# Performance work log

Hardware: AMD Instinct MI355X
Metric: run time of the kernel (lower is better)

Reference implementation:

```python
import jax, jax.numpy as jnp
import numpy as np

SEQ, EMB, QKV = 4096, 1024, 1024

def setup_inputs() -> dict:
    key = jax.random.key(0)
    k_x, k_q, k_k, k_v = jax.random.split(key, 4)
    scale = 1.0 / np.sqrt(EMB)
    return {
        "x": jax.random.normal(k_x, (SEQ, EMB), dtype=jnp.float32),
        "W_q": jax.random.normal(k_q, (EMB, QKV), dtype=jnp.float32) * scale,
        "W_k": jax.random.normal(k_k, (EMB, QKV), dtype=jnp.float32) * scale,
        "W_v": jax.random.normal(k_v, (EMB, QKV), dtype=jnp.float32) * scale,
    }

def reference(x, W_q, W_k, W_v):
    # Single-head scaled dot-product attention, unbatched: x [S, E]
    d_k = W_q.shape[1]
    Q = x @ W_q          # [S, D]
    K = x @ W_k          # [S, D]
    V = x @ W_v          # [S, D]
    scores = (Q @ K.T) * (1.0 / jnp.sqrt(jnp.asarray(d_k, dtype=x.dtype)))  # [S, S]
    attn = jax.nn.softmax(scores, axis=-1)
    return attn @ V      # [S, D]
```

## Files before the change

kernel.cpp:

```cpp
#include <hip/hip_runtime.h>
#include <cstdint>

#define S_DIM 4096
#define E_DIM 1024
#define D_DIM 1024

typedef __bf16 bf16x8 __attribute__((ext_vector_type(8)));
typedef float  f32x4  __attribute__((ext_vector_type(4)));
typedef unsigned short u16x8 __attribute__((ext_vector_type(8)));

__device__ __forceinline__ unsigned short f2bf(float f) {
  unsigned u = __float_as_uint(f);
  unsigned r = (u + 0x7fffu + ((u >> 16) & 1u)) >> 16;
  return (unsigned short)r;
}

__device__ __forceinline__ void lds_copy16(const unsigned short* g, const unsigned short* l) {
  auto gp = reinterpret_cast<__attribute__((address_space(1))) unsigned int*>(
      reinterpret_cast<uintptr_t>(g));
  auto lp = reinterpret_cast<__attribute__((address_space(3))) unsigned int*>(
      reinterpret_cast<uintptr_t>(l));
  __builtin_amdgcn_global_load_lds(gp, lp, 16, 0, 0);
}

__global__ __launch_bounds__(256) void prep_kernel(
    const float* __restrict__ x,
    const float* __restrict__ Wq, const float* __restrict__ Wk, const float* __restrict__ Wv,
    unsigned short* __restrict__ xbf, unsigned short* __restrict__ Wt,
    float* __restrict__ lsum) {
  const int z = blockIdx.z;
  const int tid = threadIdx.x;
  if (z < 3) {
    const float* W = (z == 0) ? Wq : (z == 1 ? Wk : Wv);
    unsigned short* out = Wt + (size_t)z * E_DIM * D_DIM;
    __shared__ unsigned short tile[32][33];
    int bc = blockIdx.x * 32, br = blockIdx.y * 32;
    int tx = tid & 31, ty = tid >> 5;
#pragma unroll
    for (int i = 0; i < 32; i += 8)
      tile[ty + i][tx] = f2bf(W[(size_t)(br + ty + i) * D_DIM + bc + tx]);
    __syncthreads();
#pragma unroll
    for (int i = 0; i < 32; i += 8)
      out[(size_t)(bc + ty + i) * E_DIM + br + tx] = tile[tx][ty + i];
  } else {
    int bid = blockIdx.y * 32 + blockIdx.x;
    int i = (bid * 256 + tid) * 16;
#pragma unroll
    for (int h = 0; h < 2; h++) {
      float4 a = *(const float4*)(x + i + h * 8);
      float4 b = *(const float4*)(x + i + h * 8 + 4);
      u16x8 o;
      o[0] = f2bf(a.x); o[1] = f2bf(a.y); o[2] = f2bf(a.z); o[3] = f2bf(a.w);
      o[4] = f2bf(b.x); o[5] = f2bf(b.y); o[6] = f2bf(b.z); o[7] = f2bf(b.w);
      *(u16x8*)(xbf + i + h * 8) = o;
    }
    if (bid < 16) lsum[bid * 256 + tid] = 0.f;
  }
}

__global__ __launch_bounds__(256) void transpose_bf16_kernel(
    const unsigned short* __restrict__ in, unsigned short* __restrict__ out,
    int ldin, int ldout) {
  __shared__ unsigned short tile[32][33];
  int bc = blockIdx.x * 32, br = blockIdx.y * 32;
  int tx = threadIdx.x & 31, ty = threadIdx.x >> 5;
#pragma unroll
  for (int i = 0; i < 32; i += 8)
    tile[ty + i][tx] = in[(size_t)(br + ty + i) * ldin + bc + tx];
  __syncthreads();
#pragma unroll
  for (int i = 0; i < 32; i += 8)
    out[(size_t)(bc + ty + i) * ldout + br + tx] = tile[tx][ty + i];
}

template <int MODE, bool SPLIT3>
__global__ __launch_bounds__(256, 2) void gemm_bt_kernel(
    const unsigned short* __restrict__ A, int lda,
    const unsigned short* __restrict__ Bt, int ldb,
    void* __restrict__ Cp, unsigned short* __restrict__ C1,
    unsigned short* __restrict__ C2, int ldc,
    int Kper, float scale, float* __restrict__ lsum) {
  __shared__ __align__(16) unsigned short sA[128 * 64];
  __shared__ __align__(16) unsigned short sB[128 * 64];

  const int tid = threadIdx.x;

  int flat = blockIdx.y * gridDim.x + blockIdx.x;
  int numInG = 8 * gridDim.x;
  int g = flat / numInG;
  int r = flat - g * numInG;
  const int bm = (g * 8 + (r & 7)) * 128;
  const int bn = (r >> 3) * 128;

  const int wave = tid >> 6;
  const int lane = tid & 63;
  const int q    = lane >> 4;
  const int l16  = lane & 15;
  const int wm   = (wave >> 1) * 64;
  const int wn   = (wave & 1) * 64;

  f32x4 zero = {0.f, 0.f, 0.f, 0.f};
  f32x4 acc[4][4];
#pragma unroll
  for (int t = 0; t < 4; t++)
#pragma unroll
    for (int u = 0; u < 4; u++) acc[t][u] = zero;

  const int srow   = tid >> 3;
  const int schunk = (tid & 7) ^ (srow & 3);
  const int kbase  = blockIdx.z * Kper;
  const unsigned short* ap = A  + (size_t)(bm + srow) * lda + kbase + schunk * 8;
  const unsigned short* bp = Bt + (size_t)(bn + srow) * ldb + kbase + schunk * 8;
  unsigned short* saw = sA + wave * 512;
  unsigned short* sbw = sB + wave * 512;
  const size_t stepA = (size_t)32 * lda;
  const size_t stepB = (size_t)32 * ldb;

  const int sw = (q ^ (l16 & 3)) * 8;

  for (int k0 = 0; k0 < Kper; k0 += 64) {
#pragma unroll
    for (int p = 0; p < 4; p++) {
      lds_copy16(ap + k0 + p * stepA, saw + p * 2048);
      lds_copy16(bp + k0 + p * stepB, sbw + p * 2048);
    }
    __syncthreads();

#pragma unroll
    for (int h = 0; h < 2; h++) {
      bf16x8 af[4], bfv[4];
#pragma unroll
      for (int t = 0; t < 4; t++)
        af[t] = *reinterpret_cast<const bf16x8*>(sA + (wm + t * 16 + l16) * 64 + h * 32 + sw);
#pragma unroll
      for (int u = 0; u < 4; u++)
        bfv[u] = *reinterpret_cast<const bf16x8*>(sB + (wn + u * 16 + l16) * 64 + h * 32 + sw);
#pragma unroll
      for (int t = 0; t < 4; t++)
#pragma unroll
        for (int u = 0; u < 4; u++)
          acc[t][u] = __builtin_amdgcn_mfma_f32_16x16x32_bf16(af[t], bfv[u], acc[t][u], 0, 0, 0);
    }
    __syncthreads();
  }

  unsigned short* cb16 = (unsigned short*)Cp;
  int coloff = bn;
  if constexpr (SPLIT3) {
    int which = bn >> 10;
    cb16 = (which == 0) ? (unsigned short*)Cp : (which == 1 ? C1 : C2);
    coloff = bn & 1023;
  }

#pragma unroll
  for (int t = 0; t < 4; t++) {
#pragma unroll
    for (int rr = 0; rr < 4; rr++) {
      const int row = bm + wm + t * 16 + q * 4 + rr;
      float invl = 1.0f;
      if constexpr (MODE == 2) invl = 1.0f / lsum[row];
      float rs = 0.f;
#pragma unroll
      for (int u = 0; u < 4; u++) {
        const int col = coloff + wn + u * 16 + l16;
        float v = acc[t][u][rr] * scale;
        if constexpr (MODE == 0) {
          cb16[(size_t)row * ldc + col] = f2bf(v);
        } else if constexpr (MODE == 1) {
          float p = __expf(v - 8.0f);
          rs += p;
          cb16[(size_t)row * ldc + col] = f2bf(p);
        } else {
          unsafeAtomicAdd((float*)Cp + (size_t)row * ldc + col, acc[t][u][rr] * invl);
        }
      }
      if constexpr (MODE == 1) {
        rs += __shfl_xor(rs, 1);
        rs += __shfl_xor(rs, 2);
        rs += __shfl_xor(rs, 4);
        rs += __shfl_xor(rs, 8);
        if (l16 == 0) unsafeAtomicAdd(&lsum[row], rs);
      }
    }
  }
}

extern "C" void kernel_launch(void* const* d_in, const int* in_sizes, int n_in,
                              void* d_out, int out_size, void* d_ws, size_t ws_size,
                              hipStream_t stream) {
  const float* x  = (const float*)d_in[0];
  const float* Wq = (const float*)d_in[1];
  const float* Wk = (const float*)d_in[2];
  const float* Wv = (const float*)d_in[3];
  float* out = (float*)d_out;

  char* ws = (char*)d_ws;
  const size_t MB = 1024 * 1024;
  unsigned short* SP   = (unsigned short*)(ws);
  unsigned short* Vtmp = (unsigned short*)(ws);
  unsigned short* xbf  = (unsigned short*)(ws + 8 * MB);
  unsigned short* Wt   = (unsigned short*)(ws + 16 * MB);
  unsigned short* Qbf  = (unsigned short*)(ws + 32 * MB);
  unsigned short* Kbf  = (unsigned short*)(ws + 40 * MB);
  unsigned short* Vt   = (unsigned short*)(ws + 48 * MB);
  float*          lsum = (float*)(ws + 56 * MB);

  dim3 blk(256);

  dim3 prgrid(32, 32, 4);
  prep_kernel<<<prgrid, blk, 0, stream>>>(x, Wq, Wk, Wv, xbf, Wt, lsum);

  dim3 pgrid(24, 32, 1);
  gemm_bt_kernel<0, true><<<pgrid, blk, 0, stream>>>(
      xbf, E_DIM, Wt, E_DIM, Qbf, Kbf, Vtmp, D_DIM, E_DIM, 1.0f, nullptr);

  dim3 vtgrid(32, 128);
  transpose_bf16_kernel<<<vtgrid, blk, 0, stream>>>(Vtmp, Vt, D_DIM, S_DIM);

  dim3 sgrid(32, 32, 1);
  gemm_bt_kernel<1, false><<<sgrid, blk, 0, stream>>>(
      Qbf, D_DIM, Kbf, D_DIM, SP, nullptr, nullptr, S_DIM, D_DIM, 0.03125f, lsum);

  hipMemsetAsync(out, 0, (size_t)S_DIM * D_DIM * sizeof(float), stream);
  dim3 ogrid(8, 32, 2);
  gemm_bt_kernel<2, false><<<ogrid, blk, 0, stream>>>(
      SP, S_DIM, Vt, S_DIM, out, nullptr, nullptr, D_DIM, S_DIM / 2, 1.0f, lsum);
}
```

Before: 228.1 us.

## Double-buffer GEMM LDS tiles and fuse V transpose into projection epilogue

The GEMM main loop switches from a single 64-wide K tile to two 32-wide LDS buffers, issuing async global-to-LDS loads for the next tile before computing on the current one. Partial vmcnt waits and raw s_barrier replace __syncthreads. Separately, the QKV projection epilogue writes the V block directly transposed into Vt using packed 4-element stores, which removes the standalone transpose kernel and its extra round trip through memory. The cost is halved work per barrier interval and hand-written waitcnt logic that must match the number of loads in flight.

```diff
diff --git a/kernel.cpp b/kernel.cpp
--- a/kernel.cpp
+++ b/kernel.cpp
@@ -8,6 +8,7 @@
 typedef __bf16 bf16x8 __attribute__((ext_vector_type(8)));
 typedef float  f32x4  __attribute__((ext_vector_type(4)));
 typedef unsigned short u16x8 __attribute__((ext_vector_type(8)));
+typedef unsigned short u16x4 __attribute__((ext_vector_type(4)));
 
 __device__ __forceinline__ unsigned short f2bf(float f) {
   unsigned u = __float_as_uint(f);
@@ -59,21 +60,6 @@
   }
 }
 
-__global__ __launch_bounds__(256) void transpose_bf16_kernel(
-    const unsigned short* __restrict__ in, unsigned short* __restrict__ out,
-    int ldin, int ldout) {
-  __shared__ unsigned short tile[32][33];
-  int bc = blockIdx.x * 32, br = blockIdx.y * 32;
-  int tx = threadIdx.x & 31, ty = threadIdx.x >> 5;
-#pragma unroll
-  for (int i = 0; i < 32; i += 8)
-    tile[ty + i][tx] = in[(size_t)(br + ty + i) * ldin + bc + tx];
-  __syncthreads();
-#pragma unroll
-  for (int i = 0; i < 32; i += 8)
-    out[(size_t)(bc + ty + i) * ldout + br + tx] = tile[tx][ty + i];
-}
-
 template <int MODE, bool SPLIT3>
 __global__ __launch_bounds__(256, 2) void gemm_bt_kernel(
     const unsigned short* __restrict__ A, int lda,
@@ -81,8 +67,8 @@
     void* __restrict__ Cp, unsigned short* __restrict__ C1,
     unsigned short* __restrict__ C2, int ldc,
     int Kper, float scale, float* __restrict__ lsum) {
-  __shared__ __align__(16) unsigned short sA[128 * 64];
-  __shared__ __align__(16) unsigned short sB[128 * 64];
+  __shared__ __align__(16) unsigned short sA[2][128 * 32];
+  __shared__ __align__(16) unsigned short sB[2][128 * 32];
 
   const int tid = threadIdx.x;
 
@@ -107,50 +93,76 @@
 #pragma unroll
     for (int u = 0; u < 4; u++) acc[t][u] = zero;
 
-  const int srow   = tid >> 3;
-  const int schunk = (tid & 7) ^ (srow & 3);
+  const int srow   = tid >> 2;
+  const int schunk = (tid & 3) ^ (srow & 3);
   const int kbase  = blockIdx.z * Kper;
   const unsigned short* ap = A  + (size_t)(bm + srow) * lda + kbase + schunk * 8;
   const unsigned short* bp = Bt + (size_t)(bn + srow) * ldb + kbase + schunk * 8;
-  unsigned short* saw = sA + wave * 512;
-  unsigned short* sbw = sB + wave * 512;
-  const size_t stepA = (size_t)32 * lda;
-  const size_t stepB = (size_t)32 * ldb;
+  const int wslot = wave * 512;
+  const size_t skipA = (size_t)64 * lda;
+  const size_t skipB = (size_t)64 * ldb;
 
   const int sw = (q ^ (l16 & 3)) * 8;
 
-  for (int k0 = 0; k0 < Kper; k0 += 64) {
-#pragma unroll
-    for (int p = 0; p < 4; p++) {
-      lds_copy16(ap + k0 + p * stepA, saw + p * 2048);
-      lds_copy16(bp + k0 + p * stepB, sbw + p * 2048);
-    }
-    __syncthreads();
-
-#pragma unroll
-    for (int h = 0; h < 2; h++) {
-      bf16x8 af[4], bfv[4];
-#pragma unroll
-      for (int t = 0; t < 4; t++)
-        af[t] = *reinterpret_cast<const bf16x8*>(sA + (wm + t * 16 + l16) * 64 + h * 32 + sw);
+  lds_copy16(ap, sA[0] + wslot);
+  lds_copy16(ap + skipA, sA[0] + wslot + 2048);
+  lds_copy16(bp, sB[0] + wslot);
+  lds_copy16(bp + skipB, sB[0] + wslot + 2048);
+
+  int b = 0;
+  for (int k0 = 0; k0 < Kper; k0 += 32, b ^= 1) {
+    if (k0 + 32 < Kper) {
+      const int nb = b ^ 1;
+      lds_copy16(ap + k0 + 32,         sA[nb] + wslot);
+      lds_copy16(ap + k0 + 32 + skipA, sA[nb] + wslot + 2048);
+      lds_copy16(bp + k0 + 32,         sB[nb] + wslot);
+      lds_copy16(bp + k0 + 32 + skipB, sB[nb] + wslot + 2048);
+      asm volatile("s_waitcnt vmcnt(4)\n\ts_barrier" ::: "memory");
+    } else {
+      asm volatile("s_waitcnt vmcnt(0)\n\ts_barrier" ::: "memory");
+    }
+
+    bf16x8 af[4], bfv[4];
+#pragma unroll
+    for (int t = 0; t < 4; t++)
+      af[t] = *reinterpret_cast<const bf16x8*>(sA[b] + (wm + t * 16 + l16) * 32 + sw);
+#pragma unroll
+    for (int u = 0; u < 4; u++)
+      bfv[u] = *reinterpret_cast<const bf16x8*>(sB[b] + (wn + u * 16 + l16) * 32 + sw);
+#pragma unroll
+    for (int t = 0; t < 4; t++)
 #pragma unroll
       for (int u = 0; u < 4; u++)
-        bfv[u] = *reinterpret_cast<const bf16x8*>(sB + (wn + u * 16 + l16) * 64 + h * 32 + sw);
-#pragma unroll
-      for (int t = 0; t < 4; t++)
-#pragma unroll
-        for (int u = 0; u < 4; u++)
-          acc[t][u] = __builtin_amdgcn_mfma_f32_16x16x32_bf16(af[t], bfv[u], acc[t][u], 0, 0, 0);
-    }
-    __syncthreads();
+        acc[t][u] = __builtin_amdgcn_mfma_f32_16x16x32_bf16(af[t], bfv[u], acc[t][u], 0, 0, 0);
+
+    if (k0 + 32 < Kper)
+      asm volatile("s_barrier" ::: "memory");
   }
 
   unsigned short* cb16 = (unsigned short*)Cp;
   int coloff = bn;
+  bool vtrans = false;
   if constexpr (SPLIT3) {
     int which = bn >> 10;
-    cb16 = (which == 0) ? (unsigned short*)Cp : (which == 1 ? C1 : C2);
+    vtrans = (which == 2);
+    cb16 = (which == 0) ? (unsigned short*)Cp : C1;
     coloff = bn & 1023;
+  }
+
+  if (SPLIT3 && vtrans) {
+#pragma unroll
+    for (int t = 0; t < 4; t++) {
+#pragma unroll
+      for (int u = 0; u < 4; u++) {
+        const int row0 = bm + wm + t * 16 + q * 4;
+        const int col  = coloff + wn + u * 16 + l16;
+        u16x4 pk;
+#pragma unroll
+        for (int rr = 0; rr < 4; rr++) pk[rr] = f2bf(acc[t][u][rr]);
+        *(u16x4*)(C2 + (size_t)col * S_DIM + row0) = pk;
+      }
+    }
+    return;
   }
 
 #pragma unroll
@@ -198,7 +210,6 @@
   char* ws = (char*)d_ws;
   const size_t MB = 1024 * 1024;
   unsigned short* SP   = (unsigned short*)(ws);
-  unsigned short* Vtmp = (unsigned short*)(ws);
   unsigned short* xbf  = (unsigned short*)(ws + 8 * MB);
   unsigned short* Wt   = (unsigned short*)(ws + 16 * MB);
   unsigned short* Qbf  = (unsigned short*)(ws + 32 * MB);
@@ -213,10 +224,7 @@
 
   dim3 pgrid(24, 32, 1);
   gemm_bt_kernel<0, true><<<pgrid, blk, 0, stream>>>(
-      xbf, E_DIM, Wt, E_DIM, Qbf, Kbf, Vtmp, D_DIM, E_DIM, 1.0f, nullptr);
-
-  dim3 vtgrid(32, 128);
-  transpose_bf16_kernel<<<vtgrid, blk, 0, stream>>>(Vtmp, Vt, D_DIM, S_DIM);
+      xbf, E_DIM, Wt, E_DIM, Qbf, Kbf, Vt, D_DIM, E_DIM, 1.0f, nullptr);
 
   dim3 sgrid(32, 32, 1);
   gemm_bt_kernel<1, false><<<sgrid, blk, 0, stream>>>(
```

New measurement: 234.0 us. 1.03x slower.
